# Optimization experiments

Measured on AMD Instinct MI355X. Metric: run time of the kernel, lower is better.

The kernel has to match this reference:

```python
import jax, jax.numpy as jnp
import numpy as np

T, B, INP, HID, OUT = 512, 256, 128, 256, 64
DT = 0.1   # self.dt
CPL = 0.1  # coupling_strength

def _lin(v, W, b):
    # nn.Linear: v @ W.T + b, W has shape (out, in)
    return v @ W.T + b

def setup_inputs() -> dict:
    key = jax.random.key(0)
    ks = jax.random.split(key, 20)
    def W(k, o, i, gain=0.5):
        return (jax.random.normal(k, (o, i), jnp.float32) * gain / np.sqrt(i)).astype(jnp.float32)
    z = lambda n: jnp.zeros((n,), jnp.float32)
    return {
        "x": jax.random.normal(ks[0], (T, B, INP), jnp.float32),
        "W_h_w": W(ks[1], HID, HID), "W_h_b": z(HID),
        "U_h_w": W(ks[2], HID, INP), "U_h_b": z(HID),
        "W_tau_h_w": W(ks[3], HID, HID, 0.1), "W_tau_h_b": z(HID),
        "b_h": z(HID),
        "W_z_real_w": W(ks[4], HID, HID), "W_z_real_b": z(HID),
        "W_z_imag_w": W(ks[5], HID, HID), "W_z_imag_b": z(HID),
        "U_z_w": W(ks[6], HID, INP), "U_z_b": z(HID),
        "W_tau_z_w": W(ks[7], HID, HID, 0.1), "W_tau_z_b": z(HID),
        "b_z_real": z(HID), "b_z_imag": z(HID),
        "h2z_w": W(ks[8], HID, HID, 1.0), "h2z_b": jax.random.normal(ks[9], (HID,), jnp.float32) * 0.01,
        "z2h_w": W(ks[10], HID, HID, 1.0), "z2h_b": jax.random.normal(ks[11], (HID,), jnp.float32) * 0.01,
        "out_h_w": W(ks[12], OUT, HID, 1.0), "out_h_b": jax.random.normal(ks[13], (OUT,), jnp.float32) * 0.01,
        "out_z_w": W(ks[14], OUT, HID, 1.0), "out_z_b": jax.random.normal(ks[15], (OUT,), jnp.float32) * 0.01,
    }

def reference(x, W_h_w, W_h_b, U_h_w, U_h_b, W_tau_h_w, W_tau_h_b, b_h,
              W_z_real_w, W_z_real_b, W_z_imag_w, W_z_imag_b, U_z_w, U_z_b,
              W_tau_z_w, W_tau_z_b, b_z_real, b_z_imag,
              h2z_w, h2z_b, z2h_w, z2h_b, out_h_w, out_h_b, out_z_w, out_z_b):
    # Complex state z is carried as (zr, zi) real pair; math is identical to
    # torch.complex handling (coupling uses z.real, tau_z uses |z|).
    def step(carry, x_t):
        h, zr, zi = carry
        # dh/dt (uses old h, old z -- matches torch loop ordering)
        tau_h = jnp.clip(jax.nn.sigmoid(_lin(h, W_tau_h_w, W_tau_h_b)), 0.01, 1.0) + 1e-6
        dh = (-h + jnp.tanh(_lin(h, W_h_w, W_h_b)) + _lin(x_t, U_h_w, U_h_b)
              + b_h + CPL * _lin(zr, z2h_w, z2h_b)) / tau_h
        # dz/dt (uses old h, old z)
        zabs = jnp.sqrt(zr * zr + zi * zi + 1e-24)  # |z|, eps for grad safety at 0
        tau_z = jnp.clip(jax.nn.sigmoid(_lin(zabs, W_tau_z_w, W_tau_z_b)), 0.01, 1.0) + 1e-6
        uzx = _lin(x_t, U_z_w, U_z_b)
        ch = CPL * _lin(h, h2z_w, h2z_b)
        dzr = (-zr + jnp.tanh(_lin(zr, W_z_real_w, W_z_real_b)) + uzx + b_z_real + ch) / tau_z
        dzi = (-zi + jnp.tanh(_lin(zi, W_z_imag_w, W_z_imag_b)) + uzx + b_z_imag + ch) / tau_z
        h_n = h + DT * dh
        zr_n = zr + DT * dzr
        zi_n = zi + DT * dzi
        y = _lin(h_n, out_h_w, out_h_b) + _lin(zr_n, out_z_w, out_z_b)
        return (h_n, zr_n, zi_n), y
    z0 = jnp.zeros((B, HID), x.dtype)
    _, y = jax.lax.scan(step, (z0, z0, z0), x)
    return y  # (T, B, OUT)
```

## Files before the change

kernel.cpp:

```cpp
#include <hip/hip_runtime.h>
#include <hip/hip_bf16.h>
#include <math.h>

#define T_    512
#define B_    256
#define INP_  128
#define HID_  256
#define OUT_  64
#define DT_   0.1f
#define CPL_  0.1f

typedef __attribute__((ext_vector_type(8))) short          bf16x8;
typedef __attribute__((ext_vector_type(4))) float          f32x4;
typedef __attribute__((ext_vector_type(4))) unsigned short u16x4;

#define G_WH    0
#define G_WTAUH 1
#define G_WZR   2
#define G_WZI   3
#define G_WTAUZ 4
#define G_H2Z   5
#define G_Z2H   6
#define UH     458752
#define UZ     491520
#define OH     524288
#define OZ     540672
#define NW_TOTAL 557056
#define BIAS_OFF_BYTES (NW_TOTAL * 2)
#define BT_H    0
#define BTAU_H  256
#define BH_TOT  512
#define BT_ZR   768
#define BT_ZI   1024
#define BTAU_Z  1280
#define BZR_TOT 1536
#define BZI_TOT 1792
#define BY      2048
#define FLAGS_OFF_BYTES (BIAS_OFF_BYTES + 8448)
#define STATE_OFF_BYTES (FLAGS_OFF_BYTES + 32768)

__device__ __forceinline__ unsigned short f2bf(float f) {
    unsigned int u = __float_as_uint(f);
    u += 0x7fffu + ((u >> 16) & 1u);
    return (unsigned short)(u >> 16);
}

__device__ __forceinline__ float rcp_(float x) { return __builtin_amdgcn_rcpf(x); }
__device__ __forceinline__ float sigmoid_fast(float x) {
    return rcp_(1.0f + __expf(-x));
}
__device__ __forceinline__ float tanh_fast(float x) {
    return 1.0f - 2.0f * rcp_(__expf(2.0f * x) + 1.0f);
}

__global__ void prep_weights(const float* __restrict__ Wh,   const float* __restrict__ Wtauh,
                             const float* __restrict__ Wzr,  const float* __restrict__ Wzi,
                             const float* __restrict__ Wtauz,const float* __restrict__ h2z,
                             const float* __restrict__ z2h,  const float* __restrict__ Uh,
                             const float* __restrict__ Uz,   const float* __restrict__ oh,
                             const float* __restrict__ oz,   unsigned short* __restrict__ ws) {
    int fid = blockIdx.x * 256 + threadIdx.x;
    if (fid >= NW_TOTAL / 8) return;
    int o = fid * 8;
    const float* src;
    int row, col, K;
    float scale = 1.0f;
    if (o < UH) {
        int g  = o >> 16;
        int r  = o & 65535;
        int T  = r >> 12;
        int r2 = r & 4095;
        int kt = r2 >> 9;
        int l  = (r2 & 511) >> 3;
        row = T * 16 + (l & 15);
        col = kt * 32 + (l >> 4) * 8;
        K = 256;
        if      (g == G_WH)    src = Wh;
        else if (g == G_WTAUH) src = Wtauh;
        else if (g == G_WZR)   src = Wzr;
        else if (g == G_WZI)   src = Wzi;
        else if (g == G_WTAUZ) src = Wtauz;
        else if (g == G_H2Z)   { src = h2z; scale = CPL_; }
        else                   { src = z2h; scale = CPL_; }
    } else if (o < OH) {
        int g  = (o - UH) >> 15;
        int r  = (o - UH) & 32767;
        int T  = r >> 11;
        int r2 = r & 2047;
        int kt = r2 >> 9;
        int l  = (r2 & 511) >> 3;
        row = T * 16 + (l & 15);
        col = kt * 32 + (l >> 4) * 8;
        K = 128;
        src = g ? Uz : Uh;
    } else {
        int g  = (o - OH) >> 14;
        int r  = (o - OH) & 16383;
        int T  = r >> 12;
        int r2 = r & 4095;
        int kt = r2 >> 9;
        int l  = (r2 & 511) >> 3;
        row = T * 16 + (l & 15);
        col = kt * 32 + (l >> 4) * 8;
        K = 256;
        src = g ? oz : oh;
    }
    const float* p = src + (size_t)row * K + col;
    float4 v0 = *(const float4*)p;
    float4 v1 = *(const float4*)(p + 4);
    u16x4 a, b;
    a.x = f2bf(v0.x * scale); a.y = f2bf(v0.y * scale);
    a.z = f2bf(v0.z * scale); a.w = f2bf(v0.w * scale);
    b.x = f2bf(v1.x * scale); b.y = f2bf(v1.y * scale);
    b.z = f2bf(v1.z * scale); b.w = f2bf(v1.w * scale);
    *(u16x4*)(ws + o)     = a;
    *(u16x4*)(ws + o + 4) = b;
}

__global__ void prep_bias(const float* __restrict__ Whb,  const float* __restrict__ Wtauhb,
                          const float* __restrict__ Uhb,  const float* __restrict__ bh,
                          const float* __restrict__ z2hb, const float* __restrict__ Wzrb,
                          const float* __restrict__ Wzib, const float* __restrict__ Wtauzb,
                          const float* __restrict__ Uzb,  const float* __restrict__ bzr,
                          const float* __restrict__ bzi,  const float* __restrict__ h2zb,
                          const float* __restrict__ ohb,  const float* __restrict__ ozb,
                          float* __restrict__ bias) {
    int n = threadIdx.x;
    if (n < 256) {
        bias[BT_H + n]    = Whb[n];
        bias[BTAU_H + n]  = Wtauhb[n];
        bias[BH_TOT + n]  = Uhb[n] + bh[n] + CPL_ * z2hb[n];
        bias[BT_ZR + n]   = Wzrb[n];
        bias[BT_ZI + n]   = Wzib[n];
        bias[BTAU_Z + n]  = Wtauzb[n];
        bias[BZR_TOT + n] = Uzb[n] + bzr[n] + CPL_ * h2zb[n];
        bias[BZI_TOT + n] = Uzb[n] + bzi[n] + CPL_ * h2zb[n];
        if (n < 64) bias[BY + n] = ohb[n] + ozb[n];
    }
}

__global__ void prep_zero(unsigned long long* __restrict__ p) {
    int i = blockIdx.x * 512 + threadIdx.x;
    if (i < 69632) p[i] = 0;
}

template<int NKT>
__device__ __forceinline__ void wload(bf16x8* w, const unsigned short* __restrict__ p, int loff) {
#pragma unroll
    for (int kt = 0; kt < NKT; ++kt) w[kt] = *(const bf16x8*)(p + kt * 512 + loff);
}

template<int NKT>
__device__ __forceinline__ void wgemm(const bf16x8* a, const bf16x8* w, f32x4& acc) {
#pragma unroll
    for (int kt = 0; kt < NKT; ++kt)
        acc = __builtin_amdgcn_mfma_f32_16x16x32_bf16(a[kt], w[kt], acc, 0, 0, 0);
}

__device__ __forceinline__ bf16x8 loadXfrag(const float* __restrict__ xrow, int off) {
    float4 v0 = *(const float4*)(xrow + off);
    float4 v1 = *(const float4*)(xrow + off + 4);
    bf16x8 r;
    r[0] = (short)f2bf(v0.x); r[1] = (short)f2bf(v0.y);
    r[2] = (short)f2bf(v0.z); r[3] = (short)f2bf(v0.w);
    r[4] = (short)f2bf(v1.x); r[5] = (short)f2bf(v1.y);
    r[6] = (short)f2bf(v1.z); r[7] = (short)f2bf(v1.w);
    return r;
}

__device__ __forceinline__ void loadAimg(const char* st, int m16, int hi, bf16x8* a) {
    const unsigned long long* b = (const unsigned long long*)
        (st + ((hi >> 1) * 512 + m16 * 32 + (hi & 1) * 16));
#pragma unroll
    for (int kt = 0; kt < 8; ++kt) {
        union { unsigned long long q[2]; bf16x8 v; } u;
        u.q[0] = __hip_atomic_load(b + kt * 128,     __ATOMIC_RELAXED,
                                   __HIP_MEMORY_SCOPE_AGENT);
        u.q[1] = __hip_atomic_load(b + kt * 128 + 1, __ATOMIC_RELAXED,
                                   __HIP_MEMORY_SCOPE_AGENT);
        a[kt] = u.v;
    }
}

__device__ __forceinline__ void pub_rm(char* gslot, int m16, int hi, const float* v) {
    const int odd = m16 & 1;
    float oth[4];
#pragma unroll
    for (int j = 0; j < 4; ++j) oth[j] = __shfl_xor(v[j], 1);
#pragma unroll
    for (int k = 0; k < 2; ++k) {
        const int j = odd * 2 + k;
        const int r = hi * 4 + j;
        unsigned a = f2bf(v[j]), b = f2bf(oth[j]);
        unsigned u = odd ? (b | (a << 16)) : (a | (b << 16));
        __hip_atomic_store((unsigned*)(gslot + r * 32 + (m16 & ~1) * 2), u,
                           __ATOMIC_RELAXED, __HIP_MEMORY_SCOPE_AGENT);
    }
}

__device__ __forceinline__ void waitflags(const unsigned* flg, int lane, unsigned tgt) {
    for (;;) {
        unsigned v = tgt;
        if (lane < 32)
            v = __hip_atomic_load(flg + lane * 16, __ATOMIC_RELAXED,
                                  __HIP_MEMORY_SCOPE_AGENT);
        if (__all((int)(v >= tgt))) break;
        __builtin_amdgcn_s_sleep(1);
    }
}

__device__ __forceinline__ void postflag(unsigned* myflag, int lane, unsigned val) {
    asm volatile("s_waitcnt vmcnt(0)" ::: "memory");
    if (lane == 0)
        __hip_atomic_store(myflag, val, __ATOMIC_RELAXED, __HIP_MEMORY_SCOPE_AGENT);
}

__launch_bounds__(256, 1)
__global__ void twistor_main(const float* __restrict__ x, unsigned short* __restrict__ ws,
                             float* __restrict__ y) {
    const int tid  = threadIdx.x;
    const int lane = tid & 63;
    const int w    = tid >> 6;
    const int half = w >> 1;
    const int role = w & 1;
    const int m16  = lane & 15;
    const int hi   = lane >> 4;
    const int loff = lane * 8;
    const int bid  = blockIdx.x;
    const int rg   = bid & 15;
    const int cg   = bid >> 4;
    const int tt   = cg * 2 + half;
    const int brow0 = rg * 16;
    const int n    = tt * 16 + m16;
    const float* bias = (const float*)((const char*)ws + BIAS_OFF_BYTES);
    unsigned* flg    = (unsigned*)((char*)ws + FLAGS_OFF_BYTES) + rg * 512;
    unsigned* myflag = flg + (tt * 2 + role) * 16;
    char* simg = (char*)ws + STATE_OFF_BYTES;

    bf16x8 wA[8], wB[8], wC[8], wU[4];
    bf16x8 wO[8], wO2[8];
    bf16x8 wTZ[8];
    if (role == 0) {
        wload<8>(wA, ws + G_WH    * 65536 + tt * 4096, loff);
        wload<8>(wB, ws + G_WTAUH * 65536 + tt * 4096, loff);
        wload<8>(wC, ws + G_Z2H   * 65536 + tt * 4096, loff);
        wload<4>(wU, ws + UH + tt * 2048, loff);
        if (tt < 4) {
            wload<8>(wO,  ws + OH + tt * 4096, loff);
            wload<8>(wO2, ws + OZ + tt * 4096, loff);
        }
    } else {
        wload<8>(wA, ws + G_WZR   * 65536 + tt * 4096, loff);
        wload<8>(wB, ws + G_WZI   * 65536 + tt * 4096, loff);
        wload<8>(wC, ws + G_H2Z   * 65536 + tt * 4096, loff);
        wload<4>(wU, ws + UZ + tt * 2048, loff);
        wload<8>(wTZ, ws + G_WTAUZ * 65536 + tt * 4096, loff);
    }

    const float bthh = bias[BT_H + n],    btauh = bias[BTAU_H + n], bht = bias[BH_TOT + n];
    const float btzr = bias[BT_ZR + n],   btzi  = bias[BT_ZI + n],  btauz = bias[BTAU_Z + n];
    const float bzrt = bias[BZR_TOT + n], bzit  = bias[BZI_TOT + n];
    const float by_  = (tt < 4 && role == 0) ? bias[BY + n] : 0.f;

    float s0_[4] = {0, 0, 0, 0};
    float s1_[4] = {0, 0, 0, 0};

    for (int t = 0; t < T_; ++t) {
        bf16x8 ax[4];
        {
            const float* xrow = x + ((size_t)t * B_ + brow0 + m16) * INP_;
#pragma unroll
            for (int kt = 0; kt < 4; ++kt) ax[kt] = loadXfrag(xrow, kt * 32 + hi * 8);
        }
        if (t > 0) waitflags(flg, lane, (unsigned)t);

        const char* imgR = simg + (size_t)((t & 1) * 16 + rg) * 32768;
        char*       imgW = simg + (size_t)(((t + 1) & 1) * 16 + rg) * 32768;

        bf16x8 ah[8], azr[8];
        loadAimg(imgR,        m16, hi, ah);
        loadAimg(imgR + 8192, m16, hi, azr);

        if (role == 0) {
            const bool ydo = (tt < 4) && (t > 0);
            f32x4 a_y = {0.f, 0.f, 0.f, 0.f};
            if (ydo) { wgemm<8>(ah, wO, a_y); wgemm<8>(azr, wO2, a_y); }
            f32x4 a_th = {0.f, 0.f, 0.f, 0.f}, a_tau = {0.f, 0.f, 0.f, 0.f};
            f32x4 a_ch = {0.f, 0.f, 0.f, 0.f};
            wgemm<8>(ah,  wA, a_th);
            wgemm<8>(ah,  wB, a_tau);
            wgemm<8>(azr, wC, a_ch);
            wgemm<4>(ax,  wU, a_ch);
            if (ydo) {
#pragma unroll
                for (int j = 0; j < 4; ++j)
                    y[((size_t)(t - 1) * B_ + brow0 + hi * 4 + j) * OUT_ + n] =
                        a_y[j] + by_;
            }
            float hn[4];
#pragma unroll
            for (int j = 0; j < 4; ++j) {
                float th = fminf(fmaxf(sigmoid_fast(a_tau[j] + btauh), 0.01f), 1.0f) + 1e-6f;
                float dh = -s0_[j] + tanh_fast(a_th[j] + bthh) + a_ch[j] + bht;
                hn[j]    = s0_[j] + DT_ * dh * rcp_(th);
                s0_[j] = hn[j];
            }
            pub_rm(imgW + tt * 512, m16, hi, hn);
        } else {
            bf16x8 azi[8], aza[8];
            loadAimg(imgR + 16384, m16, hi, azi);
            loadAimg(imgR + 24576, m16, hi, aza);
            f32x4 a_tzr = {0.f, 0.f, 0.f, 0.f}, a_tzi = {0.f, 0.f, 0.f, 0.f};
            f32x4 a_tz  = {0.f, 0.f, 0.f, 0.f}, a_cz  = {0.f, 0.f, 0.f, 0.f};
            wgemm<8>(azr, wA,  a_tzr);
            wgemm<8>(ah,  wC,  a_cz);
            wgemm<8>(azi, wB,  a_tzi);
            wgemm<8>(aza, wTZ, a_tz);
            wgemm<4>(ax,  wU,  a_cz);
            float zrn[4], zin[4], zan[4];
#pragma unroll
            for (int j = 0; j < 4; ++j) {
                float tz  = fminf(fmaxf(sigmoid_fast(a_tz[j] + btauz), 0.01f), 1.0f) + 1e-6f;
                float rtz = rcp_(tz);
                float dzr = -s0_[j] + tanh_fast(a_tzr[j] + btzr) + a_cz[j] + bzrt;
                float dzi = -s1_[j] + tanh_fast(a_tzi[j] + btzi) + a_cz[j] + bzit;
                zrn[j] = s0_[j] + DT_ * dzr * rtz;
                zin[j] = s1_[j] + DT_ * dzi * rtz;
                zan[j] = sqrtf(zrn[j] * zrn[j] + zin[j] * zin[j] + 1e-24f);
                s0_[j] = zrn[j]; s1_[j] = zin[j];
            }
            pub_rm(imgW + 8192  + tt * 512, m16, hi, zrn);
            pub_rm(imgW + 16384 + tt * 512, m16, hi, zin);
            pub_rm(imgW + 24576 + tt * 512, m16, hi, zan);
        }
        postflag(myflag, lane, (unsigned)(t + 1));
    }

    if (role == 0 && tt < 4) {
        waitflags(flg, lane, (unsigned)T_);
        const char* imgR = simg + (size_t)((T_ & 1) * 16 + rg) * 32768;
        bf16x8 ah[8], azr[8];
        loadAimg(imgR,        m16, hi, ah);
        loadAimg(imgR + 8192, m16, hi, azr);
        f32x4 a_y = {0.f, 0.f, 0.f, 0.f};
        wgemm<8>(ah,  wO,  a_y);
        wgemm<8>(azr, wO2, a_y);
#pragma unroll
        for (int j = 0; j < 4; ++j)
            y[((size_t)(T_ - 1) * B_ + brow0 + hi * 4 + j) * OUT_ + n] = a_y[j] + by_;
    }
}

extern "C" void kernel_launch(void* const* d_in, const int* in_sizes, int n_in,
                              void* d_out, int out_size, void* d_ws, size_t ws_size,
                              hipStream_t stream) {
    const float* x = (const float*)d_in[0];
    unsigned short* ws = (unsigned short*)d_ws;
    float* bias = (float*)((char*)d_ws + BIAS_OFF_BYTES);

    prep_weights<<<(NW_TOTAL / 8 + 255) / 256, 256, 0, stream>>>(
        (const float*)d_in[1],
        (const float*)d_in[5],
        (const float*)d_in[8],
        (const float*)d_in[10],
        (const float*)d_in[14],
        (const float*)d_in[18],
        (const float*)d_in[20],
        (const float*)d_in[3],
        (const float*)d_in[12],
        (const float*)d_in[22],
        (const float*)d_in[24],
        ws);
    prep_bias<<<1, 256, 0, stream>>>(
        (const float*)d_in[2],
        (const float*)d_in[6],
        (const float*)d_in[4],
        (const float*)d_in[7],
        (const float*)d_in[21],
        (const float*)d_in[9],
        (const float*)d_in[11],
        (const float*)d_in[15],
        (const float*)d_in[13],
        (const float*)d_in[16],
        (const float*)d_in[17],
        (const float*)d_in[19],
        (const float*)d_in[23],
        (const float*)d_in[25],
        bias);
    prep_zero<<<136, 512, 0, stream>>>(
        (unsigned long long*)((char*)d_ws + FLAGS_OFF_BYTES));
    twistor_main<<<128, 256, 0, stream>>>(x, ws, (float*)d_out);
}
```

Before: 2.903 ms.

## Replace flag barriers with poison-sentinel polling on per-timestep state slots

Adds a polling variant in which every timestep writes its state to a fresh slot that was pre-filled with a NaN poison pattern. Consumers spin on the data itself until no poison remains, so the separate flag store and flag wait (with their vmcnt drain) per step go away. The cost is a large workspace region (513 slots of 32KB per row group, roughly 270MB) that a prep kernel has to fill each call, plus heavier polling traffic. The old flag path is kept as a fallback when the workspace is too small.

```diff
diff --git a/kernel.cpp b/kernel.cpp
--- a/kernel.cpp
+++ b/kernel.cpp
@@ -36,8 +36,9 @@
 #define BZR_TOT 1536
 #define BZI_TOT 1792
 #define BY      2048
-#define FLAGS_OFF_BYTES (BIAS_OFF_BYTES + 8448)
-#define STATE_OFF_BYTES (FLAGS_OFF_BYTES + 32768)
+#define REGION_OFF_BYTES (BIAS_OFF_BYTES + 8448)
+#define POISON32 0x7FC07FC0u
+#define POISON64 0x7FC07FC07FC07FC0ull
 
 __device__ __forceinline__ unsigned short f2bf(float f) {
     unsigned int u = __float_as_uint(f);
@@ -52,6 +53,9 @@
 __device__ __forceinline__ float tanh_fast(float x) {
     return 1.0f - 2.0f * rcp_(__expf(2.0f * x) + 1.0f);
 }
+
+#define AGLD(p) __hip_atomic_load((p), __ATOMIC_RELAXED, __HIP_MEMORY_SCOPE_AGENT)
+#define AGST(p, v) __hip_atomic_store((p), (v), __ATOMIC_RELAXED, __HIP_MEMORY_SCOPE_AGENT)
 
 __global__ void prep_weights(const float* __restrict__ Wh,   const float* __restrict__ Wtauh,
                              const float* __restrict__ Wzr,  const float* __restrict__ Wzi,
@@ -139,9 +143,17 @@
     }
 }
 
+__global__ void prep_poison(unsigned long long* __restrict__ p) {
+    const size_t nslot0 = 16ull * 4096;
+    const size_t ntot   = 513ull * 16 * 4096;
+    for (size_t i = (size_t)blockIdx.x * 512 + threadIdx.x; i < ntot;
+         i += (size_t)gridDim.x * 512)
+        p[i] = (i < nslot0) ? 0ull : POISON64;
+}
+
 __global__ void prep_zero(unsigned long long* __restrict__ p) {
     int i = blockIdx.x * 512 + threadIdx.x;
-    if (i < 69632) p[i] = 0;
+    if (i < 135168) p[i] = 0;
 }
 
 template<int NKT>
@@ -174,11 +186,78 @@
 #pragma unroll
     for (int kt = 0; kt < 8; ++kt) {
         union { unsigned long long q[2]; bf16x8 v; } u;
-        u.q[0] = __hip_atomic_load(b + kt * 128,     __ATOMIC_RELAXED,
-                                   __HIP_MEMORY_SCOPE_AGENT);
-        u.q[1] = __hip_atomic_load(b + kt * 128 + 1, __ATOMIC_RELAXED,
-                                   __HIP_MEMORY_SCOPE_AGENT);
+        u.q[0] = AGLD(b + kt * 128);
+        u.q[1] = AGLD(b + kt * 128 + 1);
         a[kt] = u.v;
+    }
+}
+
+__device__ __forceinline__ int chkq(unsigned long long q) {
+    return ((unsigned)q == POISON32) || ((unsigned)(q >> 32) == POISON32);
+}
+
+__device__ __forceinline__ void pollA2(const char* slot, int m16, int hi,
+                                       bf16x8* a0, bf16x8* a1) {
+    const size_t off = (size_t)((hi >> 1) * 512 + m16 * 32 + (hi & 1) * 16);
+    const unsigned long long* b0 = (const unsigned long long*)(slot + off);
+    const unsigned long long* b1 = (const unsigned long long*)(slot + 8192 + off);
+    unsigned long long q0[16], q1[16];
+    for (;;) {
+        int dirty = 0;
+#pragma unroll
+        for (int kt = 0; kt < 8; ++kt) {
+            q0[2 * kt]     = AGLD(b0 + kt * 128);
+            q0[2 * kt + 1] = AGLD(b0 + kt * 128 + 1);
+            q1[2 * kt]     = AGLD(b1 + kt * 128);
+            q1[2 * kt + 1] = AGLD(b1 + kt * 128 + 1);
+        }
+#pragma unroll
+        for (int i = 0; i < 16; ++i) dirty |= chkq(q0[i]) | chkq(q1[i]);
+        if (!__any(dirty)) break;
+        __builtin_amdgcn_s_sleep(1);
+    }
+#pragma unroll
+    for (int kt = 0; kt < 8; ++kt) {
+        union { unsigned long long q[2]; bf16x8 v; } u;
+        u.q[0] = q0[2 * kt]; u.q[1] = q0[2 * kt + 1]; a0[kt] = u.v;
+        u.q[0] = q1[2 * kt]; u.q[1] = q1[2 * kt + 1]; a1[kt] = u.v;
+    }
+}
+
+__device__ __forceinline__ void pollA4(const char* slot, int m16, int hi,
+                                       bf16x8* a0, bf16x8* a1, bf16x8* a2, bf16x8* a3) {
+    const size_t off = (size_t)((hi >> 1) * 512 + m16 * 32 + (hi & 1) * 16);
+    const unsigned long long* b0 = (const unsigned long long*)(slot + off);
+    const unsigned long long* b1 = (const unsigned long long*)(slot + 8192 + off);
+    const unsigned long long* b2 = (const unsigned long long*)(slot + 16384 + off);
+    const unsigned long long* b3 = (const unsigned long long*)(slot + 24576 + off);
+    unsigned long long q0[16], q1[16], q2[16], q3[16];
+    for (;;) {
+        int dirty = 0;
+#pragma unroll
+        for (int kt = 0; kt < 8; ++kt) {
+            q0[2 * kt]     = AGLD(b0 + kt * 128);
+            q0[2 * kt + 1] = AGLD(b0 + kt * 128 + 1);
+            q1[2 * kt]     = AGLD(b1 + kt * 128);
+            q1[2 * kt + 1] = AGLD(b1 + kt * 128 + 1);
+            q2[2 * kt]     = AGLD(b2 + kt * 128);
+            q2[2 * kt + 1] = AGLD(b2 + kt * 128 + 1);
+            q3[2 * kt]     = AGLD(b3 + kt * 128);
+            q3[2 * kt + 1] = AGLD(b3 + kt * 128 + 1);
+        }
+#pragma unroll
+        for (int i = 0; i < 16; ++i)
+            dirty |= chkq(q0[i]) | chkq(q1[i]) | chkq(q2[i]) | chkq(q3[i]);
+        if (!__any(dirty)) break;
+        __builtin_amdgcn_s_sleep(1);
+    }
+#pragma unroll
+    for (int kt = 0; kt < 8; ++kt) {
+        union { unsigned long long q[2]; bf16x8 v; } u;
+        u.q[0] = q0[2 * kt]; u.q[1] = q0[2 * kt + 1]; a0[kt] = u.v;
+        u.q[0] = q1[2 * kt]; u.q[1] = q1[2 * kt + 1]; a1[kt] = u.v;
+        u.q[0] = q2[2 * kt]; u.q[1] = q2[2 * kt + 1]; a2[kt] = u.v;
+        u.q[0] = q3[2 * kt]; u.q[1] = q3[2 * kt + 1]; a3[kt] = u.v;
     }
 }
 
@@ -193,30 +272,12 @@
         const int r = hi * 4 + j;
         unsigned a = f2bf(v[j]), b = f2bf(oth[j]);
         unsigned u = odd ? (b | (a << 16)) : (a | (b << 16));
-        __hip_atomic_store((unsigned*)(gslot + r * 32 + (m16 & ~1) * 2), u,
-                           __ATOMIC_RELAXED, __HIP_MEMORY_SCOPE_AGENT);
-    }
-}
-
-__device__ __forceinline__ void waitflags(const unsigned* flg, int lane, unsigned tgt) {
-    for (;;) {
-        unsigned v = tgt;
-        if (lane < 32)
-            v = __hip_atomic_load(flg + lane * 16, __ATOMIC_RELAXED,
-                                  __HIP_MEMORY_SCOPE_AGENT);
-        if (__all((int)(v >= tgt))) break;
-        __builtin_amdgcn_s_sleep(1);
-    }
-}
-
-__device__ __forceinline__ void postflag(unsigned* myflag, int lane, unsigned val) {
-    asm volatile("s_waitcnt vmcnt(0)" ::: "memory");
-    if (lane == 0)
-        __hip_atomic_store(myflag, val, __ATOMIC_RELAXED, __HIP_MEMORY_SCOPE_AGENT);
+        AGST((unsigned*)(gslot + r * 32 + (m16 & ~1) * 2), u);
+    }
 }
 
 __launch_bounds__(256, 1)
-__global__ void twistor_main(const float* __restrict__ x, unsigned short* __restrict__ ws,
+__global__ void twistor_poll(const float* __restrict__ x, unsigned short* __restrict__ ws,
                              float* __restrict__ y) {
     const int tid  = threadIdx.x;
     const int lane = tid & 63;
@@ -233,9 +294,148 @@
     const int brow0 = rg * 16;
     const int n    = tt * 16 + m16;
     const float* bias = (const float*)((const char*)ws + BIAS_OFF_BYTES);
-    unsigned* flg    = (unsigned*)((char*)ws + FLAGS_OFF_BYTES) + rg * 512;
+    char* simg = (char*)ws + REGION_OFF_BYTES;
+
+    bf16x8 wA[8], wB[8], wC[8], wU[4];
+    bf16x8 wO[8], wO2[8];
+    bf16x8 wTZ[8];
+    if (role == 0) {
+        wload<8>(wA, ws + G_WH    * 65536 + tt * 4096, loff);
+        wload<8>(wB, ws + G_WTAUH * 65536 + tt * 4096, loff);
+        wload<8>(wC, ws + G_Z2H   * 65536 + tt * 4096, loff);
+        wload<4>(wU, ws + UH + tt * 2048, loff);
+        if (tt < 4) {
+            wload<8>(wO,  ws + OH + tt * 4096, loff);
+            wload<8>(wO2, ws + OZ + tt * 4096, loff);
+        }
+    } else {
+        wload<8>(wA, ws + G_WZR   * 65536 + tt * 4096, loff);
+        wload<8>(wB, ws + G_WZI   * 65536 + tt * 4096, loff);
+        wload<8>(wC, ws + G_H2Z   * 65536 + tt * 4096, loff);
+        wload<4>(wU, ws + UZ + tt * 2048, loff);
+        wload<8>(wTZ, ws + G_WTAUZ * 65536 + tt * 4096, loff);
+    }
+
+    const float bthh = bias[BT_H + n],    btauh = bias[BTAU_H + n], bht = bias[BH_TOT + n];
+    const float btzr = bias[BT_ZR + n],   btzi  = bias[BT_ZI + n],  btauz = bias[BTAU_Z + n];
+    const float bzrt = bias[BZR_TOT + n], bzit  = bias[BZI_TOT + n];
+    const float by_  = (tt < 4 && role == 0) ? bias[BY + n] : 0.f;
+
+    float s0_[4] = {0, 0, 0, 0};
+    float s1_[4] = {0, 0, 0, 0};
+
+    for (int t = 0; t < T_; ++t) {
+        bf16x8 ax[4];
+        {
+            const float* xrow = x + ((size_t)t * B_ + brow0 + m16) * INP_;
+#pragma unroll
+            for (int kt = 0; kt < 4; ++kt) ax[kt] = loadXfrag(xrow, kt * 32 + hi * 8);
+        }
+        const char* slotR = simg + ((size_t)t * 16 + rg) * 32768;
+        char*       slotW = simg + ((size_t)(t + 1) * 16 + rg) * 32768;
+
+        if (role == 0) {
+            bf16x8 ah[8], azr[8];
+            pollA2(slotR, m16, hi, ah, azr);
+            const bool ydo = (tt < 4) && (t > 0);
+            f32x4 a_y = {0.f, 0.f, 0.f, 0.f};
+            if (ydo) { wgemm<8>(ah, wO, a_y); wgemm<8>(azr, wO2, a_y); }
+            f32x4 a_th = {0.f, 0.f, 0.f, 0.f}, a_tau = {0.f, 0.f, 0.f, 0.f};
+            f32x4 a_ch = {0.f, 0.f, 0.f, 0.f};
+            wgemm<8>(ah,  wA, a_th);
+            wgemm<8>(ah,  wB, a_tau);
+            wgemm<8>(azr, wC, a_ch);
+            wgemm<4>(ax,  wU, a_ch);
+            if (ydo) {
+#pragma unroll
+                for (int j = 0; j < 4; ++j)
+                    y[((size_t)(t - 1) * B_ + brow0 + hi * 4 + j) * OUT_ + n] =
+                        a_y[j] + by_;
+            }
+            float hn[4];
+#pragma unroll
+            for (int j = 0; j < 4; ++j) {
+                float th = fminf(fmaxf(sigmoid_fast(a_tau[j] + btauh), 0.01f), 1.0f) + 1e-6f;
+                float dh = -s0_[j] + tanh_fast(a_th[j] + bthh) + a_ch[j] + bht;
+                hn[j]    = s0_[j] + DT_ * dh * rcp_(th);
+                s0_[j] = hn[j];
+            }
+            pub_rm(slotW + tt * 512, m16, hi, hn);
+        } else {
+            bf16x8 ah[8], azr[8], azi[8], aza[8];
+            pollA4(slotR, m16, hi, ah, azr, azi, aza);
+            f32x4 a_tzr = {0.f, 0.f, 0.f, 0.f}, a_tzi = {0.f, 0.f, 0.f, 0.f};
+            f32x4 a_tz  = {0.f, 0.f, 0.f, 0.f}, a_cz  = {0.f, 0.f, 0.f, 0.f};
+            wgemm<8>(azr, wA,  a_tzr);
+            wgemm<8>(ah,  wC,  a_cz);
+            wgemm<8>(azi, wB,  a_tzi);
+            wgemm<8>(aza, wTZ, a_tz);
+            wgemm<4>(ax,  wU,  a_cz);
+            float zrn[4], zin[4], zan[4];
+#pragma unroll
+            for (int j = 0; j < 4; ++j) {
+                float tz  = fminf(fmaxf(sigmoid_fast(a_tz[j] + btauz), 0.01f), 1.0f) + 1e-6f;
+                float rtz = rcp_(tz);
+                float dzr = -s0_[j] + tanh_fast(a_tzr[j] + btzr) + a_cz[j] + bzrt;
+                float dzi = -s1_[j] + tanh_fast(a_tzi[j] + btzi) + a_cz[j] + bzit;
+                zrn[j] = s0_[j] + DT_ * dzr * rtz;
+                zin[j] = s1_[j] + DT_ * dzi * rtz;
+                zan[j] = sqrtf(zrn[j] * zrn[j] + zin[j] * zin[j] + 1e-24f);
+                s0_[j] = zrn[j]; s1_[j] = zin[j];
+            }
+            pub_rm(slotW + 8192  + tt * 512, m16, hi, zrn);
+            pub_rm(slotW + 16384 + tt * 512, m16, hi, zin);
+            pub_rm(slotW + 24576 + tt * 512, m16, hi, zan);
+        }
+    }
+
+    if (role == 0 && tt < 4) {
+        const char* slotR = simg + ((size_t)T_ * 16 + rg) * 32768;
+        bf16x8 ah[8], azr[8];
+        pollA2(slotR, m16, hi, ah, azr);
+        f32x4 a_y = {0.f, 0.f, 0.f, 0.f};
+        wgemm<8>(ah,  wO,  a_y);
+        wgemm<8>(azr, wO2, a_y);
+#pragma unroll
+        for (int j = 0; j < 4; ++j)
+            y[((size_t)(T_ - 1) * B_ + brow0 + hi * 4 + j) * OUT_ + n] = a_y[j] + by_;
+    }
+}
+
+__device__ __forceinline__ void waitflags(const unsigned* flg, int lane, unsigned tgt) {
+    for (;;) {
+        unsigned v = tgt;
+        if (lane < 32) v = AGLD(flg + lane * 16);
+        if (__all((int)(v >= tgt))) break;
+        __builtin_amdgcn_s_sleep(1);
+    }
+}
+__device__ __forceinline__ void postflag(unsigned* myflag, int lane, unsigned val) {
+    asm volatile("s_waitcnt vmcnt(0)" ::: "memory");
+    if (lane == 0) AGST(myflag, val);
+}
+
+__launch_bounds__(256, 1)
+__global__ void twistor_flag(const float* __restrict__ x, unsigned short* __restrict__ ws,
+                             float* __restrict__ y) {
+    const int tid  = threadIdx.x;
+    const int lane = tid & 63;
+    const int w    = tid >> 6;
+    const int half = w >> 1;
+    const int role = w & 1;
+    const int m16  = lane & 15;
+    const int hi   = lane >> 4;
+    const int loff = lane * 8;
+    const int bid  = blockIdx.x;
+    const int rg   = bid & 15;
+    const int cg   = bid >> 4;
+    const int tt   = cg * 2 + half;
+    const int brow0 = rg * 16;
+    const int n    = tt * 16 + m16;
+    const float* bias = (const float*)((const char*)ws + BIAS_OFF_BYTES);
+    unsigned* flg    = (unsigned*)((char*)ws + REGION_OFF_BYTES) + rg * 512;
     unsigned* myflag = flg + (tt * 2 + role) * 16;
-    char* simg = (char*)ws + STATE_OFF_BYTES;
+    char* simg = (char*)ws + REGION_OFF_BYTES + 32768;
 
     bf16x8 wA[8], wB[8], wC[8], wU[4];
     bf16x8 wO[8], wO2[8];
@@ -387,7 +587,15 @@
         (const float*)d_in[23],
         (const float*)d_in[25],
         bias);
-    prep_zero<<<136, 512, 0, stream>>>(
-        (unsigned long long*)((char*)d_ws + FLAGS_OFF_BYTES));
-    twistor_main<<<128, 256, 0, stream>>>(x, ws, (float*)d_out);
-}
+
+    const size_t pollNeed = (size_t)REGION_OFF_BYTES + 513ull * 16 * 32768;
+    if (ws_size >= pollNeed) {
+        prep_poison<<<8192, 512, 0, stream>>>(
+            (unsigned long long*)((char*)d_ws + REGION_OFF_BYTES));
+        twistor_poll<<<128, 256, 0, stream>>>(x, ws, (float*)d_out);
+    } else {
+        prep_zero<<<264, 512, 0, stream>>>(
+            (unsigned long long*)((char*)d_ws + REGION_OFF_BYTES));
+        twistor_flag<<<128, 256, 0, stream>>>(x, ws, (float*)d_out);
+    }
+}
```

After: 2.657 ms. 8.5% less time.
